# Performance work log

Hardware: AMD Instinct MI355X
Metric: run time of the kernel (lower is better)

## Reference

```python
import jax, jax.numpy as jnp
import numpy as np

NB, BS, NHID, NINP = 6, 200, 1200, 2400  # num_blocks, block_size, nhid, ninp (=2*nhid)
T, B, NTOK = 32, 32, 16000


def _ln(x, g, b):
    mu = x.mean(-1, keepdims=True)
    v = ((x - mu) ** 2).mean(-1, keepdims=True)
    return (x - mu) / jnp.sqrt(v + 1e-5) * g + b


def _attend(q3, k3, v3, wq, wk, wv, wfc, g, b, nh, dk, dv, residual):
    # q3/k3/v3: (B, L, d_model); multi-head scaled-dot attention across blocks
    Bz, L, _ = q3.shape
    qh = (q3 @ wq).reshape(Bz, L, nh, dk)
    kh = (k3 @ wk).reshape(Bz, L, nh, dk)
    vh = (v3 @ wv).reshape(Bz, L, nh, dv)
    att = jnp.einsum('bqhd,bkhd->bhqk', qh, kh) / float(np.sqrt(dk))
    att = jax.nn.softmax(att, axis=-1)
    out = jnp.einsum('bhqk,bkhd->bqhd', att, vh).reshape(Bz, L, nh * dv)
    out = out @ wfc
    if residual:
        out = out + q3
    return _ln(out, g, b)


def setup_inputs() -> dict:
    key = jax.random.key(0)
    ks = jax.random.split(key, 16)
    rn = lambda i, sh, s: jax.random.normal(ks[i], sh, dtype=jnp.float32) * s
    d = {}
    d['tokens'] = jax.random.randint(ks[0], (T, B), 0, NTOK)
    d['h0'] = jnp.zeros((2, B, NHID), jnp.float32)
    d['c0'] = jnp.zeros((2, B, NHID), jnp.float32)
    d['emb_table'] = jax.random.uniform(ks[1], (NTOK, NINP), jnp.float32, -0.1, 0.1)
    d['Wi'] = rn(2, (NB, 4 * BS, NINP), 0.01)
    d['Wh'] = rn(3, (NB, 4 * BS, BS), 0.05)
    d['bih'] = jnp.zeros((NB, 4 * BS), jnp.float32)
    d['bhh'] = jnp.zeros((NB, 4 * BS), jnp.float32)
    d['mq'] = rn(4, (BS, 64), 0.07)
    d['mk'] = rn(5, (BS, 64), 0.07)
    d['mv'] = rn(6, (BS, 64), 0.07)
    d['mfc'] = rn(7, (64, BS), 0.1)
    d['mg'] = jnp.ones((BS,), jnp.float32)
    d['mb'] = jnp.zeros((BS,), jnp.float32)
    d['lq'] = rn(8, (BS, 1600), 0.07)
    d['lk'] = rn(9, (BS, 1600), 0.07)
    d['lv'] = rn(10, (BS, 1600), 0.07)
    d['lfc'] = rn(11, (1600, 2400), 0.02)
    d['lg'] = jnp.ones((2400,), jnp.float32)
    d['lb'] = jnp.zeros((2400,), jnp.float32)
    d['dec_w'] = jax.random.uniform(ks[12], (NTOK, NHID), jnp.float32, -0.1, 0.1)
    d['dec_b'] = jnp.zeros((NTOK,), jnp.float32)
    return d


def reference(tokens, h0, c0, emb_table, Wi, Wh, bih, bhh, mq, mk, mv, mfc, mg, mb,
              lq, lk, lv, lfc, lg, lb, dec_w, dec_b):
    def block_lstm(x, h, c):
        # block-diagonal LSTMCell: k independent cells, per-block input NINP, hidden BS
        Bz = x.shape[0]
        xb = x.reshape(Bz, NB, -1)
        hb = h.reshape(Bz, NB, BS)
        cb = c.reshape(Bz, NB, BS)
        gt = jnp.einsum('bki,kgi->bkg', xb, Wi) + jnp.einsum('bkh,kgh->bkg', hb, Wh) + bih + bhh
        ii, ff, gg, oo = jnp.split(gt, 4, axis=-1)  # torch LSTMCell gate order i,f,g,o
        cn = jax.nn.sigmoid(ff) * cb + jax.nn.sigmoid(ii) * jnp.tanh(gg)
        hn = jax.nn.sigmoid(oo) * jnp.tanh(cn)
        return hn.reshape(Bz, NHID), cn.reshape(Bz, NHID)

    def self_att(h):
        hb = h.reshape(-1, NB, BS)
        hb = _attend(hb, hb, hb, mq, mk, mv, mfc, mg, mb, 4, 16, 16, True)
        return hb.reshape(-1, NHID)

    emb = emb_table[tokens]  # (T, B, NINP)

    def step0(carry, x):
        h, c = carry
        h, c = block_lstm(jnp.tile(x, (1, NB)), h, c)
        h = self_att(h)
        return (h, c), h

    (hf0, cf0), out = jax.lax.scan(step0, (h0[0], c0[0]), emb)

    def step1(carry, x):
        h, c = carry
        q = h.reshape(-1, NB, BS)
        kv = x.reshape(-1, NB, BS)
        inp = _attend(q, kv, kv, lq, lk, lv, lfc, lg, lb, 8, BS, BS, False)  # (B, NB, 2400)
        h, c = block_lstm(inp.reshape(inp.shape[0], -1), h, c)
        h = self_att(h)
        return (h, c), h

    (hf1, cf1), out = jax.lax.scan(step1, (h0[1], c0[1]), out)

    decoded = out @ dec_w.T + dec_b  # (T, B, NTOK)
    return decoded, jnp.stack([hf0, hf1]), jnp.stack([cf0, cf1])
```

## Files before the change

### kernel.cpp

```cpp
#include <hip/hip_runtime.h>
#include <math.h>

#define NBLK 6
#define BS   200
#define NHID 1200
#define NINP 2400
#define TT   32
#define BZ   32
#define NTOK 16000
#define NG   4800
#define ROWS 1024
#define L1D  1600

__device__ __forceinline__ float sigmoidf_(float x) { return 1.0f / (1.0f + expf(-x)); }

template <bool BT>
__global__ __launch_bounds__(256) void gemm128_kernel(
    const float* __restrict__ A, const float* __restrict__ B,
    const float* __restrict__ bias1, const float* __restrict__ bias2,
    float* __restrict__ C, int M, int N, int K, const int* __restrict__ a_idx)
{
    __shared__ __align__(16) float As[8][132];
    __shared__ __align__(16) float Bs[8][132];
    const int tid = threadIdx.x;
    const int tx = tid & 15, ty = tid >> 4;
    const int n0 = blockIdx.x * 128, m0 = blockIdx.y * 128;

    const int la_r = tid >> 1, la_k = (tid & 1) * 4;
    long arow;
    {
        int row = m0 + la_r;
        arow = a_idx ? (long)a_idx[row] * K : (long)row * K;
    }
    float acc[8][8] = {};

    for (int k0 = 0; k0 < K; k0 += 8) {
        {
// ... 38 lines not shown
    for (int i = 0; i < 8; i++) {
        int row = m0 + ty * 4 + (i & 3) + (i >> 2) * 64;
        #pragma unroll
        for (int jg = 0; jg < 2; jg++) {
            int col = n0 + tx * 4 + jg * 64;
            if (col < N) {
                float4 v;
                v.x = acc[i][jg * 4 + 0]; v.y = acc[i][jg * 4 + 1];
                v.z = acc[i][jg * 4 + 2]; v.w = acc[i][jg * 4 + 3];
                if (bias1) {
                    float4 b1 = *(const float4*)&bias1[col];
                    v.x += b1.x; v.y += b1.y; v.z += b1.z; v.w += b1.w;
                }
                if (bias2) {
                    float4 b2 = *(const float4*)&bias2[col];
                    v.x += b2.x; v.y += b2.y; v.z += b2.z; v.w += b2.w;
                }
                *(float4*)&C[(long)row * N + col] = v;
            }
        }
    }
}

__global__ __launch_bounds__(256) void gemm_skp_kernel(
    const float* __restrict__ A, const float* __restrict__ B,
    float* __restrict__ Cp, int M, int N, int K, int KL)
{
    __shared__ __align__(16) float As[8][68];
    __shared__ __align__(16) float Bs[8][68];
    const int tid = threadIdx.x;
    const int tx = tid & 15, ty = tid >> 4;
    const int n0 = blockIdx.x * 64, m0 = blockIdx.y * 64;
    const int z = blockIdx.z;
    const int kbeg = z * KL, kend = kbeg + KL;

    float acc[4][4] = {};

    for (int k0 = kbeg; k0 < kend; k0 += 8) {
        {
            int idx = tid * 2;
            int mm = idx >> 3, kk = idx & 7;
            int row = m0 + mm;
            float2 v = *(const float2*)&A[(long)row * K + k0 + kk];
            As[kk][mm] = v.x;
            As[kk + 1][mm] = v.y;
        }
        {
            int idx = tid * 2;
            int nn = idx & 63, kk = idx >> 6;
            int n = n0 + nn;
            float2 v = make_float2(0.f, 0.f);
            if (n < N) v = *(const float2*)&B[(long)(k0 + kk) * N + n];
            Bs[kk][nn] = v.x;
            Bs[kk][nn + 1] = v.y;
        }
        __syncthreads();
        #pragma unroll
        for (int kk = 0; kk < 8; kk++) {
            const float4 a4 = *(const float4*)&As[kk][ty * 4];
            const float4 b4 = *(const float4*)&Bs[kk][tx * 4];
            const float av[4] = {a4.x, a4.y, a4.z, a4.w};
            const float bv[4] = {b4.x, b4.y, b4.z, b4.w};
            #pragma unroll
            for (int i = 0; i < 4; i++)
                #pragma unroll
                for (int j = 0; j < 4; j++) acc[i][j] += av[i] * bv[j];
        }
        __syncthreads();
    }
    float* Cz = Cp + (long)z * M * N;
    #pragma unroll
    for (int i = 0; i < 4; i++) {
        int row = m0 + ty * 4 + i;
        #pragma unroll
        for (int j = 0; j < 4; j++) {
            int col = n0 + tx * 4 + j;
            if (col < N) Cz[(long)row * N + col] = acc[i][j];
        }
    }
}

__global__ __launch_bounds__(256) void bigb_kernel(
    const float* __restrict__ lq, const float* __restrict__ lk,
    float* __restrict__ BigB)
{
    int id = blockIdx.x * 256 + threadIdx.x;
    if (id >= 320000) return;
    int h = id / 40000, r = id % 40000, cp = r / 200, c = r % 200;
    const float4* a = (const float4*)(lq + (long)c * L1D + h * 200);
    const float4* b = (const float4*)(lk + (long)cp * L1D + h * 200);
    float s0 = 0, s1 = 0, s2 = 0, s3 = 0;
    #pragma unroll 5
    for (int d = 0; d < 50; d++) {
        float4 av = a[d], bv = b[d];
        s0 += av.x * bv.x; s1 += av.y * bv.y; s2 += av.z * bv.z; s3 += av.w * bv.w;
    }
    BigB[(long)cp * L1D + h * 200 + c] = s0 + s1 + s2 + s3;
}

__global__ __launch_bounds__(256) void lstm0_kernel(
    const float* __restrict__ GX,
    const float* __restrict__ hprev,
    float* __restrict__ c_io,
    const float* __restrict__ Wh,
    float* __restrict__ h_out)
{
    __shared__ float h_s[200 * 33];
    const int k = blockIdx.y, jt = blockIdx.x, tid = threadIdx.x;
    for (int idx = tid; idx < 1600; idx += 256) {
        int bb = idx / 50, m4 = idx % 50;
        float4 v = *(const float4*)&hprev[bb * NHID + k * BS + m4 * 4];
        h_s[(m4 * 4 + 0) * 33 + bb] = v.x;
        h_s[(m4 * 4 + 1) * 33 + bb] = v.y;
        h_s[(m4 * 4 + 2) * 33 + bb] = v.z;
        h_s[(m4 * 4 + 3) * 33 + bb] = v.w;
    }
    __syncthreads();
    const int b = tid & 31, jj = tid >> 5;
    const int j = jt * 8 + jj;
    const float* w0 = Wh + (long)(k * 800 + j) * 200;
    const float* w1 = w0 + 200 * 200;
    const float* w2 = w0 + 400 * 200;
    const float* w3 = w0 + 600 * 200;
    float a0 = 0, a1 = 0, a2 = 0, a3 = 0;
    for (int m = 0; m < 200; m += 4) {
        float4 wv0 = *(const float4*)&w0[m];
        float4 wv1 = *(const float4*)&w1[m];
        float4 wv2 = *(const float4*)&w2[m];
        float4 wv3 = *(const float4*)&w3[m];
        float h0v = h_s[(m + 0) * 33 + b];
        float h1v = h_s[(m + 1) * 33 + b];
        float h2v = h_s[(m + 2) * 33 + b];
        float h3v = h_s[(m + 3) * 33 + b];
        a0 += h0v * wv0.x + h1v * wv0.y + h2v * wv0.z + h3v * wv0.w;
        a1 += h0v * wv1.x + h1v * wv1.y + h2v * wv1.z + h3v * wv1.w;
        a2 += h0v * wv2.x + h1v * wv2.y + h2v * wv2.z + h3v * wv2.w;
        a3 += h0v * wv3.x + h1v * wv3.y + h2v * wv3.z + h3v * wv3.w;
    }
    const float* gx = GX + b * NG + k * 800;
    float gi = a0 + gx[j];
    float gf = a1 + gx[200 + j];
    float gg = a2 + gx[400 + j];
    float go = a3 + gx[600 + j];
    int o = b * NHID + k * BS + j;
    float cold = c_io[o];
    float cn = sigmoidf_(gf) * cold + sigmoidf_(gi) * tanhf(gg);
    float hn = sigmoidf_(go) * tanhf(cn);
    c_io[o] = cn;
    h_out[o] = hn;
}

__global__ __launch_bounds__(512) void lstm1_kernel(
    const float* __restrict__ inp, const float* __restrict__ hprev,
    float* __restrict__ c_io, const float* __restrict__ Wi,
    const float* __restrict__ Wh, const float* __restrict__ bih,
    const float* __restrict__ bhh, float* __restrict__ h_out)
{
    __shared__ float h_s[200 * 33];
    __shared__ float x_s[2][100 * 33];
    __shared__ float ps[12][128];
    const int k = blockIdx.y, jt = blockIdx.x, tid = threadIdx.x;
    const int b = tid & 31, jg = (tid >> 5) & 3, kh = tid >> 7;
    const int j = jt * 4 + jg;

    for (int idx = tid; idx < 1600; idx += 512) {
        int bb = idx / 50, m4 = idx % 50;
        float4 v = *(const float4*)&hprev[bb * NHID + k * BS + m4 * 4];
        h_s[(m4 * 4 + 0) * 33 + bb] = v.x;
        h_s[(m4 * 4 + 1) * 33 + bb] = v.y;
        h_s[(m4 * 4 + 2) * 33 + bb] = v.z;
        h_s[(m4 * 4 + 3) * 33 + bb] = v.w;
    }
    for (int idx = tid; idx < 800; idx += 512) {
        int bb = idx / 25, m4 = idx % 25;
        float4 v = *(const float4*)&inp[(long)(bb * 6 + k) * NINP + m4 * 4];
        x_s[0][(m4 * 4 + 0) * 33 + bb] = v.x;
        x_s[0][(m4 * 4 + 1) * 33 + bb] = v.y;
        x_s[0][(m4 * 4 + 2) * 33 + bb] = v.z;
        x_s[0][(m4 * 4 + 3) * 33 + bb] = v.w;
    }

    const float* wi0 = Wi + (long)(k * 800 + j) * NINP;
    const float* wi1 = wi0 + (long)200 * NINP;
    const float* wi2 = wi0 + (long)400 * NINP;
    const float* wi3 = wi0 + (long)600 * NINP;
    float a0 = 0, a1 = 0, a2 = 0, a3 = 0;
    int cur = 0;
    for (int ti = 0; ti < 24; ti++) {
        __syncthreads();
        if (ti + 1 < 24) {
            int kt = (ti + 1) * 100;
            float* xs = x_s[cur ^ 1];
            for (int idx = tid; idx < 800; idx += 512) {
                int bb = idx / 25, m4 = idx % 25;
                float4 v = *(const float4*)&inp[(long)(bb * 6 + k) * NINP + kt + m4 * 4];
                xs[(m4 * 4 + 0) * 33 + bb] = v.x;
                xs[(m4 * 4 + 1) * 33 + bb] = v.y;
                xs[(m4 * 4 + 2) * 33 + bb] = v.z;
                xs[(m4 * 4 + 3) * 33 + bb] = v.w;
            }
        }
        if (ti / 6 == kh) {
            const int kt = ti * 100;
            const float* xs = x_s[cur];
            for (int m = 0; m < 100; m += 4) {
                float4 w0 = *(const float4*)&wi0[kt + m];
                float4 w1 = *(const float4*)&wi1[kt + m];
                float4 w2 = *(const float4*)&wi2[kt + m];
                float4 w3 = *(const float4*)&wi3[kt + m];
                float x0 = xs[(m + 0) * 33 + b];
                float x1 = xs[(m + 1) * 33 + b];
                float x2 = xs[(m + 2) * 33 + b];
                float x3 = xs[(m + 3) * 33 + b];
                a0 += x0 * w0.x + x1 * w0.y + x2 * w0.z + x3 * w0.w;
                a1 += x0 * w1.x + x1 * w1.y + x2 * w1.z + x3 * w1.w;
                a2 += x0 * w2.x + x1 * w2.y + x2 * w2.z + x3 * w2.w;
                a3 += x0 * w3.x + x1 * w3.y + x2 * w3.z + x3 * w3.w;
            }
        }
        cur ^= 1;
    }
    if (kh == 0) {
        const float* w0 = Wh + (long)(k * 800 + j) * 200;
        const float* w1 = w0 + 200 * 200;
        const float* w2 = w0 + 400 * 200;
        const float* w3 = w0 + 600 * 200;
        for (int m = 0; m < 200; m += 4) {
            float4 wv0 = *(const float4*)&w0[m];
            float4 wv1 = *(const float4*)&w1[m];
            float4 wv2 = *(const float4*)&w2[m];
            float4 wv3 = *(const float4*)&w3[m];
            float h0v = h_s[(m + 0) * 33 + b];
            float h1v = h_s[(m + 1) * 33 + b];
            float h2v = h_s[(m + 2) * 33 + b];
            float h3v = h_s[(m + 3) * 33 + b];
            a0 += h0v * wv0.x + h1v * wv0.y + h2v * wv0.z + h3v * wv0.w;
            a1 += h0v * wv1.x + h1v * wv1.y + h2v * wv1.z + h3v * wv1.w;
            a2 += h0v * wv2.x + h1v * wv2.y + h2v * wv2.z + h3v * wv2.w;
            a3 += h0v * wv3.x + h1v * wv3.y + h2v * wv3.z + h3v * wv3.w;
        }
    } else {
        int g = (kh - 1) * 4, t = tid & 127;
        ps[g + 0][t] = a0; ps[g + 1][t] = a1; ps[g + 2][t] = a2; ps[g + 3][t] = a3;
    }
    __syncthreads();
    if (kh == 0) {
        a0 += ps[0][tid] + ps[4][tid] + ps[8][tid];
        a1 += ps[1][tid] + ps[5][tid] + ps[9][tid];
        a2 += ps[2][tid] + ps[6][tid] + ps[10][tid];
        a3 += ps[3][tid] + ps[7][tid] + ps[11][tid];
        int nb = k * 800;
        float gi = a0 + bih[nb + j] + bhh[nb + j];
        float gf = a1 + bih[nb + 200 + j] + bhh[nb + 200 + j];
        float gg = a2 + bih[nb + 400 + j] + bhh[nb + 400 + j];
        float go = a3 + bih[nb + 600 + j] + bhh[nb + 600 + j];
        int o = b * NHID + k * BS + j;
        float cold = c_io[o];
        float cn = sigmoidf_(gf) * cold + sigmoidf_(gi) * tanhf(gg);
        float hn = sigmoidf_(go) * tanhf(cn);
        c_io[o] = cn;
        h_out[o] = hn;
    }
}

__global__ __launch_bounds__(256) void att_small_kernel(
    const float* __restrict__ h_in, float* __restrict__ h_out,
    const float* __restrict__ mq, const float* __restrict__ mk,
    const float* __restrict__ mv, const float* __restrict__ mfc,
    const float* __restrict__ mg, const float* __restrict__ mb)
{
    __shared__ float hb[1200];
    __shared__ float qh[384], kh[384], vh[384];
    __shared__ float att[144];
    __shared__ float outp[384];
    __shared__ float o2[1200];
    __shared__ float mu_s[6], rs_s[6];
    const int b = blockIdx.x, tid = threadIdx.x;
    for (int i = tid; i < 300; i += 256)
        ((float4*)hb)[i] = ((const float4*)(h_in + b * NHID))[i];
    __syncthreads();
    if (tid < 192) {
        int which = tid >> 6, hd = tid & 63;
        const float* Mw = which == 0 ? mq : (which == 1 ? mk : mv);
        float acc[6] = {};
        for (int jx = 0; jx < 200; jx++) {
            float w = Mw[jx * 64 + hd];
            #pragma unroll
            for (int l = 0; l < 6; l++) acc[l] += hb[l * 200 + jx] * w;
        }
        float* dst = which == 0 ? qh : (which == 1 ? kh : vh);
        #pragma unroll
        for (int l = 0; l < 6; l++) dst[l * 64 + hd] = acc[l];
    }
    __syncthreads();
    if (tid < 144) {
        int h = tid / 36, r = tid % 36, q = r / 6, kk = r % 6;
        float s = 0;
        #pragma unroll
        for (int d = 0; d < 16; d++) s += qh[q * 64 + h * 16 + d] * kh[kk * 64 + h * 16 + d];
        att[(h * 6 + q) * 6 + kk] = s * 0.25f;
    }
    __syncthreads();
    if (tid < 24) {
        float* a = &att[tid * 6];
        float mx = a[0];
        for (int i = 1; i < 6; i++) mx = fmaxf(mx, a[i]);
        float sm = 0;
        for (int i = 0; i < 6; i++) { a[i] = expf(a[i] - mx); sm += a[i]; }
        float inv = 1.f / sm;
        for (int i = 0; i < 6; i++) a[i] *= inv;
    }
    __syncthreads();
    for (int id = tid; id < 384; id += 256) {
        int q = id >> 6, hd = id & 63, h = hd >> 4;
        float s = 0;
        #pragma unroll
        for (int kk = 0; kk < 6; kk++) s += att[(h * 6 + q) * 6 + kk] * vh[kk * 64 + hd];
        outp[id] = s;
    }
    __syncthreads();
    if (tid < 200) {
        float acc[6] = {};
        for (int d = 0; d < 64; d++) {
            float w = mfc[d * 200 + tid];
            #pragma unroll
            for (int q = 0; q < 6; q++) acc[q] += outp[q * 64 + d] * w;
        }
// ... 10 lines not shown
            s2 += v.x * v.x + v.y * v.y + v.z * v.z + v.w * v.w;
        }
        float mu = s / 200.f;
        float var = s2 / 200.f - mu * mu;
        mu_s[tid] = mu;
        rs_s[tid] = 1.0f / sqrtf(var + 1e-5f);
    }
    __syncthreads();
    for (int i = tid; i < 300; i += 256) {
        int q = i / 50;
        float4 v = ((float4*)o2)[i];
        float4 g4 = ((const float4*)mg)[i % 50];
        float4 b4 = ((const float4*)mb)[i % 50];
        float mu = mu_s[q], rstd = rs_s[q];
        float4 r;
        r.x = (v.x - mu) * rstd * g4.x + b4.x;
        r.y = (v.y - mu) * rstd * g4.y + b4.y;
        r.z = (v.z - mu) * rstd * g4.z + b4.z;
        r.w = (v.w - mu) * rstd * g4.w + b4.w;
        ((float4*)(h_out + b * NHID))[i] = r;
    }
}

__global__ __launch_bounds__(256) void att1_kernel(
    const float* __restrict__ hp,
    const float* __restrict__ KM,
    const float* __restrict__ VH,
    float* __restrict__ attV)
{
    __shared__ float att[288];
    const int b = blockIdx.x, tid = threadIdx.x;
    const float* qb = hp + b * NHID;
    const float* kb = KM + b * 9600;
    const float* vb = VH + b * 9600;
    for (int id = tid; id < 288; id += 256) {
        int h = id / 36, r = id % 36, q = r / 6, kk = r % 6;
        const float4* qr = (const float4*)(qb + q * 200);
        const float4* kr = (const float4*)(kb + kk * L1D + h * 200);
        float s0 = 0, s1 = 0, s2 = 0, s3 = 0;
        #pragma unroll 5
        for (int d = 0; d < 50; d++) {
            float4 a = qr[d], v = kr[d];
            s0 += a.x * v.x; s1 += a.y * v.y; s2 += a.z * v.z; s3 += a.w * v.w;
        }
        att[(h * 6 + q) * 6 + kk] = (s0 + s1 + s2 + s3) * 0.07071067811865475f;
    }
    __syncthreads();
    if (tid < 48) {
        float* a = &att[tid * 6];
        float mx = a[0];
        for (int i = 1; i < 6; i++) mx = fmaxf(mx, a[i]);
        float sm = 0;
        for (int i = 0; i < 6; i++) { a[i] = expf(a[i] - mx); sm += a[i]; }
        float inv = 1.f / sm;
        for (int i = 0; i < 6; i++) a[i] *= inv;
    }
    __syncthreads();
    for (int hd = tid; hd < L1D; hd += 256) {
        int h = hd / 200;
        float v0 = vb[0 * L1D + hd], v1 = vb[1 * L1D + hd], v2 = vb[2 * L1D + hd];
        float v3 = vb[3 * L1D + hd], v4 = vb[4 * L1D + hd], v5 = vb[5 * L1D + hd];
        #pragma unroll
        for (int q = 0; q < 6; q++) {
            const float* a = &att[(h * 6 + q) * 6];
            float s = a[0] * v0 + a[1] * v1 + a[2] * v2 + a[3] * v3 + a[4] * v4 + a[5] * v5;
            attV[b * 9600 + q * L1D + hd] = s;
        }
    }
}

__global__ __launch_bounds__(256) void ln_sum4_kernel(
    const float* __restrict__ Fp, float* __restrict__ Y,
    const float* __restrict__ g, const float* __restrict__ bta)
{
    __shared__ float rowbuf[2400];
    __shared__ float aw[4], bw[4];
    const int r = blockIdx.x, tid = threadIdx.x;
    const long SL = (long)192 * NINP / 4;
    const float4* f0 = (const float4*)(Fp) + (long)r * (NINP / 4);
    float s = 0, s2 = 0;
    for (int i = tid; i < 600; i += 256) {
        float4 a = f0[i], b2 = f0[SL + i], c = f0[2 * SL + i], d = f0[3 * SL + i];
        float4 v;
        v.x = a.x + b2.x + c.x + d.x;
        v.y = a.y + b2.y + c.y + d.y;
        v.z = a.z + b2.z + c.z + d.z;
        v.w = a.w + b2.w + c.w + d.w;
        ((float4*)rowbuf)[i] = v;
        s += v.x + v.y + v.z + v.w;
        s2 += v.x * v.x + v.y * v.y + v.z * v.z + v.w * v.w;
    }
    for (int off = 32; off; off >>= 1) { s += __shfl_down(s, off); s2 += __shfl_down(s2, off); }
    int wid = tid >> 6, lane = tid & 63;
    if (lane == 0) { aw[wid] = s; bw[wid] = s2; }
    __syncthreads();
    if (tid == 0) {
        float a = 0, a2 = 0;
        for (int w = 0; w < 4; w++) { a += aw[w]; a2 += bw[w]; }
        float mu = a / NINP;
        float var = a2 / NINP - mu * mu;
        aw[0] = mu;
        bw[0] = 1.0f / sqrtf(var + 1e-5f);
    }
    __syncthreads();
    float mu = aw[0], rstd = bw[0];
    for (int i = tid; i < 600; i += 256) {
        float4 v = ((float4*)rowbuf)[i];
        float4 g4 = ((const float4*)g)[i];
        float4 b4 = ((const float4*)bta)[i];
        float4 o;
        o.x = (v.x - mu) * rstd * g4.x + b4.x;
        o.y = (v.y - mu) * rstd * g4.y + b4.y;
        o.z = (v.z - mu) * rstd * g4.z + b4.z;
        o.w = (v.w - mu) * rstd * g4.w + b4.w;
        ((float4*)(Y + (long)r * NINP))[i] = o;
    }
}

extern "C" void kernel_launch(void* const* d_in, const int* in_sizes, int n_in,
                              void* d_out, int out_size, void* d_ws, size_t ws_size,
                              hipStream_t stream)
{
    const int*   tokens = (const int*)  d_in[0];
    const float* h0     = (const float*)d_in[1];
    const float* c0     = (const float*)d_in[2];
    const float* emb    = (const float*)d_in[3];
    const float* Wi     = (const float*)d_in[4];
    const float* Wh     = (const float*)d_in[5];
    const float* bih    = (const float*)d_in[6];
    const float* bhh    = (const float*)d_in[7];
    const float* mq     = (const float*)d_in[8];
    const float* mk     = (const float*)d_in[9];
    const float* mv     = (const float*)d_in[10];
    const float* mfc    = (const float*)d_in[11];
    const float* mg     = (const float*)d_in[12];
    const float* mb     = (const float*)d_in[13];
    const float* lq     = (const float*)d_in[14];
    const float* lk     = (const float*)d_in[15];
    const float* lv     = (const float*)d_in[16];
    const float* lfc    = (const float*)d_in[17];
    const float* lg     = (const float*)d_in[18];
    const float* lb     = (const float*)d_in[19];
    const float* dec_w  = (const float*)d_in[20];
    const float* dec_b  = (const float*)d_in[21];
    float* out = (float*)d_out;

    float* p = (float*)d_ws;
    float* GX0  = p; p += (long)ROWS * NG;
    float* out0 = p; p += (long)ROWS * NHID;
    float* out1 = p; p += (long)ROWS * NHID;
    float* KM   = p; p += (long)ROWS * 6 * L1D;
    float* VH1  = p; p += (long)ROWS * 6 * L1D;
    float* attV = p; p += 192 * L1D;
    float* FCp  = p; p += (long)4 * 192 * NINP;
    float* inp  = p; p += 192 * NINP;
    float* htmp = p; p += BZ * NHID;
    float* cb0  = p; p += BZ * NHID;
    float* cb1  = p; p += BZ * NHID;
    float* BigB = p; p += 200 * L1D;

    const int ST = BZ * NHID;

    hipMemcpyAsync(cb0, c0,      ST * sizeof(float), hipMemcpyDeviceToDevice, stream);
    hipMemcpyAsync(cb1, c0 + ST, ST * sizeof(float), hipMemcpyDeviceToDevice, stream);

    bigb_kernel<<<1250, 256, 0, stream>>>(lq, lk, BigB);

    gemm128_kernel<true><<<dim3(NG / 128 + 1, ROWS / 128), 256, 0, stream>>>(
        emb, Wi, bih, bhh, GX0, ROWS, NG, NINP, tokens);

    for (int t = 0; t < TT; t++) {
        const float* hp = (t == 0) ? h0 : out0 + (t - 1) * ST;
        lstm0_kernel<<<dim3(25, 6), 256, 0, stream>>>(
            GX0 + (long)t * BZ * NG, hp, cb0, Wh, htmp);
        att_small_kernel<<<BZ, 256, 0, stream>>>(htmp, out0 + t * ST, mq, mk, mv, mfc, mg, mb);
    }

    gemm128_kernel<false><<<dim3((L1D + 127) / 128, (ROWS * 6) / 128), 256, 0, stream>>>(
        out0, BigB, nullptr, nullptr, KM, ROWS * 6, L1D, BS, nullptr);
    gemm128_kernel<false><<<dim3((L1D + 127) / 128, (ROWS * 6) / 128), 256, 0, stream>>>(
        out0, lv, nullptr, nullptr, VH1, ROWS * 6, L1D, BS, nullptr);

    for (int t = 0; t < TT; t++) {
        const float* hp = (t == 0) ? h0 + ST : out1 + (t - 1) * ST;
        att1_kernel<<<BZ, 256, 0, stream>>>(
            hp, KM + (long)t * BZ * 6 * L1D, VH1 + (long)t * BZ * 6 * L1D, attV);
        gemm_skp_kernel<<<dim3((NINP + 63) / 64, 3, 4), 256, 0, stream>>>(
            attV, lfc, FCp, 192, NINP, L1D, 400);
        ln_sum4_kernel<<<192, 256, 0, stream>>>(FCp, inp, lg, lb);
        lstm1_kernel<<<dim3(50, 6), 512, 0, stream>>>(inp, hp, cb1, Wi, Wh, bih, bhh, htmp);
        att_small_kernel<<<BZ, 256, 0, stream>>>(htmp, out1 + t * ST, mq, mk, mv, mfc, mg, mb);
    }

    gemm128_kernel<true><<<dim3(NTOK / 128, ROWS / 128), 256, 0, stream>>>(
        out1, dec_w, dec_b, nullptr, out, ROWS, NTOK, NHID, nullptr);

    long off = (long)ROWS * NTOK;
    hipMemcpyAsync(out + off,          out0 + 31 * ST, ST * sizeof(float), hipMemcpyDeviceToDevice, stream);
    hipMemcpyAsync(out + off + ST,     out1 + 31 * ST, ST * sizeof(float), hipMemcpyDeviceToDevice, stream);
    hipMemcpyAsync(out + off + 2 * ST, cb0,            ST * sizeof(float), hipMemcpyDeviceToDevice, stream);
    hipMemcpyAsync(out + off + 3 * ST, cb1,            ST * sizeof(float), hipMemcpyDeviceToDevice, stream);
}
```

Measured before the change: 10.40 ms.

## Fuse per-timestep recurrent kernels into persistent kernels with grid barriers

Replaces the per-timestep launch loops of both LSTM layers with two persistent kernels, one per phase, that step through all timesteps and use an atomic-counter grid barrier between stages. The goal is to remove roughly 224 small kernel launches and their launch gaps. The second-layer LSTM is also rebalanced to 150 blocks of 256 threads, each running the full input reduction, where before it used a 512-thread split-K reduction. This relies on every block being co-resident, or the barrier deadlocks, and blocks that have no work in a stage still pay barrier latency.

```diff
diff --git a/kernel.cpp b/kernel.cpp
--- a/kernel.cpp
+++ b/kernel.cpp
@@ -11,8 +11,27 @@
 #define NG   4800
 #define ROWS 1024
 #define L1D  1600
+#define ST   (BZ*NHID)
 
 __device__ __forceinline__ float sigmoidf_(float x) { return 1.0f / (1.0f + expf(-x)); }
+
+template <int NB>
+__device__ __forceinline__ void gbar(unsigned* bar, unsigned gen) {
+    __syncthreads();
+    if (threadIdx.x == 0) {
+        __threadfence();
+        unsigned old = __hip_atomic_fetch_add(&bar[0], 1u, __ATOMIC_ACQ_REL, __HIP_MEMORY_SCOPE_AGENT);
+        if (old == gen * (unsigned)NB - 1u) {
+            __hip_atomic_store(&bar[16], gen, __ATOMIC_RELEASE, __HIP_MEMORY_SCOPE_AGENT);
+        } else {
+            while (__hip_atomic_load(&bar[16], __ATOMIC_ACQUIRE, __HIP_MEMORY_SCOPE_AGENT) < gen) {
+                __builtin_amdgcn_s_sleep(2);
+            }
+        }
+        __threadfence();
+    }
+    __syncthreads();
+}
 
 template <bool BT>
 __global__ __launch_bounds__(256) void gemm128_kernel(
@@ -97,64 +116,6 @@
     }
 }
 
-__global__ __launch_bounds__(256) void gemm_skp_kernel(
-    const float* __restrict__ A, const float* __restrict__ B,
-    float* __restrict__ Cp, int M, int N, int K, int KL)
-{
-    __shared__ __align__(16) float As[8][68];
-    __shared__ __align__(16) float Bs[8][68];
-    const int tid = threadIdx.x;
-    const int tx = tid & 15, ty = tid >> 4;
-    const int n0 = blockIdx.x * 64, m0 = blockIdx.y * 64;
-    const int z = blockIdx.z;
-    const int kbeg = z * KL, kend = kbeg + KL;
-
-    float acc[4][4] = {};
-
-    for (int k0 = kbeg; k0 < kend; k0 += 8) {
-        {
-            int idx = tid * 2;
-            int mm = idx >> 3, kk = idx & 7;
-            int row = m0 + mm;
-            float2 v = *(const float2*)&A[(long)row * K + k0 + kk];
-            As[kk][mm] = v.x;
-            As[kk + 1][mm] = v.y;
-        }
-        {
-            int idx = tid * 2;
-            int nn = idx & 63, kk = idx >> 6;
-            int n = n0 + nn;
-            float2 v = make_float2(0.f, 0.f);
-            if (n < N) v = *(const float2*)&B[(long)(k0 + kk) * N + n];
-            Bs[kk][nn] = v.x;
-            Bs[kk][nn + 1] = v.y;
-        }
-        __syncthreads();
-        #pragma unroll
-        for (int kk = 0; kk < 8; kk++) {
-            const float4 a4 = *(const float4*)&As[kk][ty * 4];
-            const float4 b4 = *(const float4*)&Bs[kk][tx * 4];
-            const float av[4] = {a4.x, a4.y, a4.z, a4.w};
-            const float bv[4] = {b4.x, b4.y, b4.z, b4.w};
-            #pragma unroll
-            for (int i = 0; i < 4; i++)
-                #pragma unroll
-                for (int j = 0; j < 4; j++) acc[i][j] += av[i] * bv[j];
-        }
-        __syncthreads();
-    }
-    float* Cz = Cp + (long)z * M * N;
-    #pragma unroll
-    for (int i = 0; i < 4; i++) {
-        int row = m0 + ty * 4 + i;
-        #pragma unroll
-        for (int j = 0; j < 4; j++) {
-            int col = n0 + tx * 4 + j;
-            if (col < N) Cz[(long)row * N + col] = acc[i][j];
-        }
-    }
-}
-
 __global__ __launch_bounds__(256) void bigb_kernel(
     const float* __restrict__ lq, const float* __restrict__ lk,
     float* __restrict__ BigB)
@@ -173,184 +134,21 @@
     BigB[(long)cp * L1D + h * 200 + c] = s0 + s1 + s2 + s3;
 }
 
-__global__ __launch_bounds__(256) void lstm0_kernel(
-    const float* __restrict__ GX,
-    const float* __restrict__ hprev,
-    float* __restrict__ c_io,
-    const float* __restrict__ Wh,
-    float* __restrict__ h_out)
+__device__ __forceinline__ void att_small_body(
+    float* smem, const float* h_in, float* h_out, int b,
+    const float* mq, const float* mk, const float* mv, const float* mfc,
+    const float* mg, const float* mb)
 {
-    __shared__ float h_s[200 * 33];
-    const int k = blockIdx.y, jt = blockIdx.x, tid = threadIdx.x;
-    for (int idx = tid; idx < 1600; idx += 256) {
-        int bb = idx / 50, m4 = idx % 50;
-        float4 v = *(const float4*)&hprev[bb * NHID + k * BS + m4 * 4];
-        h_s[(m4 * 4 + 0) * 33 + bb] = v.x;
-        h_s[(m4 * 4 + 1) * 33 + bb] = v.y;
-        h_s[(m4 * 4 + 2) * 33 + bb] = v.z;
-        h_s[(m4 * 4 + 3) * 33 + bb] = v.w;
-    }
-    __syncthreads();
-    const int b = tid & 31, jj = tid >> 5;
-    const int j = jt * 8 + jj;
-    const float* w0 = Wh + (long)(k * 800 + j) * 200;
-    const float* w1 = w0 + 200 * 200;
-    const float* w2 = w0 + 400 * 200;
-    const float* w3 = w0 + 600 * 200;
-    float a0 = 0, a1 = 0, a2 = 0, a3 = 0;
-    for (int m = 0; m < 200; m += 4) {
-        float4 wv0 = *(const float4*)&w0[m];
-        float4 wv1 = *(const float4*)&w1[m];
-        float4 wv2 = *(const float4*)&w2[m];
-        float4 wv3 = *(const float4*)&w3[m];
-        float h0v = h_s[(m + 0) * 33 + b];
-        float h1v = h_s[(m + 1) * 33 + b];
-        float h2v = h_s[(m + 2) * 33 + b];
-        float h3v = h_s[(m + 3) * 33 + b];
-        a0 += h0v * wv0.x + h1v * wv0.y + h2v * wv0.z + h3v * wv0.w;
-        a1 += h0v * wv1.x + h1v * wv1.y + h2v * wv1.z + h3v * wv1.w;
-        a2 += h0v * wv2.x + h1v * wv2.y + h2v * wv2.z + h3v * wv2.w;
-        a3 += h0v * wv3.x + h1v * wv3.y + h2v * wv3.z + h3v * wv3.w;
-    }
-    const float* gx = GX + b * NG + k * 800;
-    float gi = a0 + gx[j];
-    float gf = a1 + gx[200 + j];
-    float gg = a2 + gx[400 + j];
-    float go = a3 + gx[600 + j];
-    int o = b * NHID + k * BS + j;
-    float cold = c_io[o];
-    float cn = sigmoidf_(gf) * cold + sigmoidf_(gi) * tanhf(gg);
-    float hn = sigmoidf_(go) * tanhf(cn);
-    c_io[o] = cn;
-    h_out[o] = hn;
-}
-
-__global__ __launch_bounds__(512) void lstm1_kernel(
-    const float* __restrict__ inp, const float* __restrict__ hprev,
-    float* __restrict__ c_io, const float* __restrict__ Wi,
-    const float* __restrict__ Wh, const float* __restrict__ bih,
-    const float* __restrict__ bhh, float* __restrict__ h_out)
-{
-    __shared__ float h_s[200 * 33];
-    __shared__ float x_s[2][100 * 33];
-    __shared__ float ps[12][128];
-    const int k = blockIdx.y, jt = blockIdx.x, tid = threadIdx.x;
-    const int b = tid & 31, jg = (tid >> 5) & 3, kh = tid >> 7;
-    const int j = jt * 4 + jg;
-
-    for (int idx = tid; idx < 1600; idx += 512) {
-        int bb = idx / 50, m4 = idx % 50;
-        float4 v = *(const float4*)&hprev[bb * NHID + k * BS + m4 * 4];
-        h_s[(m4 * 4 + 0) * 33 + bb] = v.x;
-        h_s[(m4 * 4 + 1) * 33 + bb] = v.y;
-        h_s[(m4 * 4 + 2) * 33 + bb] = v.z;
-        h_s[(m4 * 4 + 3) * 33 + bb] = v.w;
-    }
-    for (int idx = tid; idx < 800; idx += 512) {
-        int bb = idx / 25, m4 = idx % 25;
-        float4 v = *(const float4*)&inp[(long)(bb * 6 + k) * NINP + m4 * 4];
-        x_s[0][(m4 * 4 + 0) * 33 + bb] = v.x;
-        x_s[0][(m4 * 4 + 1) * 33 + bb] = v.y;
-        x_s[0][(m4 * 4 + 2) * 33 + bb] = v.z;
-        x_s[0][(m4 * 4 + 3) * 33 + bb] = v.w;
-    }
-
-    const float* wi0 = Wi + (long)(k * 800 + j) * NINP;
-    const float* wi1 = wi0 + (long)200 * NINP;
-    const float* wi2 = wi0 + (long)400 * NINP;
-    const float* wi3 = wi0 + (long)600 * NINP;
-    float a0 = 0, a1 = 0, a2 = 0, a3 = 0;
-    int cur = 0;
-    for (int ti = 0; ti < 24; ti++) {
-        __syncthreads();
-        if (ti + 1 < 24) {
-            int kt = (ti + 1) * 100;
-            float* xs = x_s[cur ^ 1];
-            for (int idx = tid; idx < 800; idx += 512) {
-                int bb = idx / 25, m4 = idx % 25;
-                float4 v = *(const float4*)&inp[(long)(bb * 6 + k) * NINP + kt + m4 * 4];
-                xs[(m4 * 4 + 0) * 33 + bb] = v.x;
-                xs[(m4 * 4 + 1) * 33 + bb] = v.y;
-                xs[(m4 * 4 + 2) * 33 + bb] = v.z;
-                xs[(m4 * 4 + 3) * 33 + bb] = v.w;
-            }
-        }
-        if (ti / 6 == kh) {
-            const int kt = ti * 100;
-            const float* xs = x_s[cur];
-            for (int m = 0; m < 100; m += 4) {
-                float4 w0 = *(const float4*)&wi0[kt + m];
-                float4 w1 = *(const float4*)&wi1[kt + m];
-                float4 w2 = *(const float4*)&wi2[kt + m];
-                float4 w3 = *(const float4*)&wi3[kt + m];
-                float x0 = xs[(m + 0) * 33 + b];
-                float x1 = xs[(m + 1) * 33 + b];
-                float x2 = xs[(m + 2) * 33 + b];
-                float x3 = xs[(m + 3) * 33 + b];
-                a0 += x0 * w0.x + x1 * w0.y + x2 * w0.z + x3 * w0.w;
-                a1 += x0 * w1.x + x1 * w1.y + x2 * w1.z + x3 * w1.w;
-                a2 += x0 * w2.x + x1 * w2.y + x2 * w2.z + x3 * w2.w;
-                a3 += x0 * w3.x + x1 * w3.y + x2 * w3.z + x3 * w3.w;
-            }
-        }
-        cur ^= 1;
-    }
-    if (kh == 0) {
-        const float* w0 = Wh + (long)(k * 800 + j) * 200;
-        const float* w1 = w0 + 200 * 200;
-        const float* w2 = w0 + 400 * 200;
-        const float* w3 = w0 + 600 * 200;
-        for (int m = 0; m < 200; m += 4) {
-            float4 wv0 = *(const float4*)&w0[m];
-            float4 wv1 = *(const float4*)&w1[m];
-            float4 wv2 = *(const float4*)&w2[m];
-            float4 wv3 = *(const float4*)&w3[m];
-            float h0v = h_s[(m + 0) * 33 + b];
-            float h1v = h_s[(m + 1) * 33 + b];
-            float h2v = h_s[(m + 2) * 33 + b];
-            float h3v = h_s[(m + 3) * 33 + b];
-            a0 += h0v * wv0.x + h1v * wv0.y + h2v * wv0.z + h3v * wv0.w;
-            a1 += h0v * wv1.x + h1v * wv1.y + h2v * wv1.z + h3v * wv1.w;
-            a2 += h0v * wv2.x + h1v * wv2.y + h2v * wv2.z + h3v * wv2.w;
-            a3 += h0v * wv3.x + h1v * wv3.y + h2v * wv3.z + h3v * wv3.w;
-        }
-    } else {
-        int g = (kh - 1) * 4, t = tid & 127;
-        ps[g + 0][t] = a0; ps[g + 1][t] = a1; ps[g + 2][t] = a2; ps[g + 3][t] = a3;
-    }
-    __syncthreads();
-    if (kh == 0) {
-        a0 += ps[0][tid] + ps[4][tid] + ps[8][tid];
-        a1 += ps[1][tid] + ps[5][tid] + ps[9][tid];
-        a2 += ps[2][tid] + ps[6][tid] + ps[10][tid];
-        a3 += ps[3][tid] + ps[7][tid] + ps[11][tid];
-        int nb = k * 800;
-        float gi = a0 + bih[nb + j] + bhh[nb + j];
-        float gf = a1 + bih[nb + 200 + j] + bhh[nb + 200 + j];
-        float gg = a2 + bih[nb + 400 + j] + bhh[nb + 400 + j];
-        float go = a3 + bih[nb + 600 + j] + bhh[nb + 600 + j];
-        int o = b * NHID + k * BS + j;
-        float cold = c_io[o];
-        float cn = sigmoidf_(gf) * cold + sigmoidf_(gi) * tanhf(gg);
-        float hn = sigmoidf_(go) * tanhf(cn);
-        c_io[o] = cn;
-        h_out[o] = hn;
-    }
-}
-
-__global__ __launch_bounds__(256) void att_small_kernel(
-    const float* __restrict__ h_in, float* __restrict__ h_out,
-    const float* __restrict__ mq, const float* __restrict__ mk,
-    const float* __restrict__ mv, const float* __restrict__ mfc,
-    const float* __restrict__ mg, const float* __restrict__ mb)
-{
-    __shared__ float hb[1200];
-    __shared__ float qh[384], kh[384], vh[384];
-    __shared__ float att[144];
-    __shared__ float outp[384];
-    __shared__ float o2[1200];
-    __shared__ float mu_s[6], rs_s[6];
-    const int b = blockIdx.x, tid = threadIdx.x;
+    const int tid = threadIdx.x;
+    float* hb   = smem;
+    float* qh   = smem + 1200;
+    float* kh   = smem + 1584;
+    float* vh   = smem + 1968;
+    float* att  = smem + 2352;
+    float* outp = smem + 2496;
+    float* o2   = smem + 2880;
+    float* mu_s = smem + 4080;
+    float* rs_s = smem + 4088;
     for (int i = tid; i < 300; i += 256)
         ((float4*)hb)[i] = ((const float4*)(h_in + b * NHID))[i];
     __syncthreads();
@@ -377,7 +175,7 @@
     }
     __syncthreads();
     if (tid < 24) {
-        float* a = &att[tid * 6];
+        float* a = att + tid * 6;
         float mx = a[0];
         for (int i = 1; i < 6; i++) mx = fmaxf(mx, a[i]);
         float sm = 0;
@@ -434,98 +232,331 @@
     }
 }
 
-__global__ __launch_bounds__(256) void att1_kernel(
-    const float* __restrict__ hp,
-    const float* __restrict__ KM,
-    const float* __restrict__ VH,
-    float* __restrict__ attV)
+#define GRID_A 160
+__global__ __launch_bounds__(256) void phaseA_kernel(
+    const float* __restrict__ GX0, const float* __restrict__ h0,
+    float* __restrict__ cb0, const float* __restrict__ Wh,
+    float* __restrict__ out0, float* __restrict__ htmp,
+    const float* __restrict__ mq, const float* __restrict__ mk,
+    const float* __restrict__ mv, const float* __restrict__ mfc,
+    const float* __restrict__ mg, const float* __restrict__ mb,
+    unsigned* bar)
 {
-    __shared__ float att[288];
-    const int b = blockIdx.x, tid = threadIdx.x;
-    const float* qb = hp + b * NHID;
-    const float* kb = KM + b * 9600;
-    const float* vb = VH + b * 9600;
-    for (int id = tid; id < 288; id += 256) {
-        int h = id / 36, r = id % 36, q = r / 6, kk = r % 6;
-        const float4* qr = (const float4*)(qb + q * 200);
-        const float4* kr = (const float4*)(kb + kk * L1D + h * 200);
-        float s0 = 0, s1 = 0, s2 = 0, s3 = 0;
-        #pragma unroll 5
-        for (int d = 0; d < 50; d++) {
-            float4 a = qr[d], v = kr[d];
-            s0 += a.x * v.x; s1 += a.y * v.y; s2 += a.z * v.z; s3 += a.w * v.w;
-        }
-        att[(h * 6 + q) * 6 + kk] = (s0 + s1 + s2 + s3) * 0.07071067811865475f;
-    }
-    __syncthreads();
-    if (tid < 48) {
-        float* a = &att[tid * 6];
-        float mx = a[0];
-        for (int i = 1; i < 6; i++) mx = fmaxf(mx, a[i]);
-        float sm = 0;
-        for (int i = 0; i < 6; i++) { a[i] = expf(a[i] - mx); sm += a[i]; }
-        float inv = 1.f / sm;
-        for (int i = 0; i < 6; i++) a[i] *= inv;
-    }
-    __syncthreads();
-    for (int hd = tid; hd < L1D; hd += 256) {
-        int h = hd / 200;
-        float v0 = vb[0 * L1D + hd], v1 = vb[1 * L1D + hd], v2 = vb[2 * L1D + hd];
-        float v3 = vb[3 * L1D + hd], v4 = vb[4 * L1D + hd], v5 = vb[5 * L1D + hd];
-        #pragma unroll
-        for (int q = 0; q < 6; q++) {
-            const float* a = &att[(h * 6 + q) * 6];
-            float s = a[0] * v0 + a[1] * v1 + a[2] * v2 + a[3] * v3 + a[4] * v4 + a[5] * v5;
-            attV[b * 9600 + q * L1D + hd] = s;
-        }
+    __shared__ __align__(16) float smem[13232];
+    const int blk = blockIdx.x, tid = threadIdx.x;
+    unsigned gen = 0;
+    for (int t = 0; t < TT; t++) {
+        const float* hp = (t == 0) ? h0 : out0 + (long)(t - 1) * ST;
+        if (blk < 150) {
+            const int k = blk / 25, jt = blk % 25;
+            float* h_s = smem;
+            for (int idx = tid; idx < 1600; idx += 256) {
+                int bb = idx / 50, m4 = idx % 50;
+                float4 v = *(const float4*)&hp[bb * NHID + k * BS + m4 * 4];
+                h_s[(m4 * 4 + 0) * 33 + bb] = v.x;
+                h_s[(m4 * 4 + 1) * 33 + bb] = v.y;
+                h_s[(m4 * 4 + 2) * 33 + bb] = v.z;
+                h_s[(m4 * 4 + 3) * 33 + bb] = v.w;
+            }
+            __syncthreads();
+            const int b = tid & 31, jj = tid >> 5;
+            const int j = jt * 8 + jj;
+            const float* w0 = Wh + (long)(k * 800 + j) * 200;
+            const float* w1 = w0 + 200 * 200;
+            const float* w2 = w0 + 400 * 200;
+            const float* w3 = w0 + 600 * 200;
+            float a0 = 0, a1 = 0, a2 = 0, a3 = 0;
+            for (int m = 0; m < 200; m += 4) {
+                float4 wv0 = *(const float4*)&w0[m];
+                float4 wv1 = *(const float4*)&w1[m];
+                float4 wv2 = *(const float4*)&w2[m];
+                float4 wv3 = *(const float4*)&w3[m];
+                float h0v = h_s[(m + 0) * 33 + b], h1v = h_s[(m + 1) * 33 + b];
+                float h2v = h_s[(m + 2) * 33 + b], h3v = h_s[(m + 3) * 33 + b];
+                a0 += h0v * wv0.x + h1v * wv0.y + h2v * wv0.z + h3v * wv0.w;
+                a1 += h0v * wv1.x + h1v * wv1.y + h2v * wv1.z + h3v * wv1.w;
+                a2 += h0v * wv2.x + h1v * wv2.y + h2v * wv2.z + h3v * wv2.w;
+                a3 += h0v * wv3.x + h1v * wv3.y + h2v * wv3.z + h3v * wv3.w;
+            }
+            const float* gx = GX0 + (long)t * BZ * NG + b * NG + k * 800;
+            float gi = a0 + gx[j];
+            float gf = a1 + gx[200 + j];
+            float gg = a2 + gx[400 + j];
+            float go = a3 + gx[600 + j];
+            int o = b * NHID + k * BS + j;
+            float cold = cb0[o];
+            float cn = sigmoidf_(gf) * cold + sigmoidf_(gi) * tanhf(gg);
+            float hn = sigmoidf_(go) * tanhf(cn);
+            cb0[o] = cn;
+            htmp[o] = hn;
+        }
+        gbar<GRID_A>(bar, ++gen);
+        if (blk < 32)
+            att_small_body(smem, htmp, out0 + (long)t * ST, blk, mq, mk, mv, mfc, mg, mb);
+        gbar<GRID_A>(bar, ++gen);
     }
 }
 
-__global__ __launch_bounds__(256) void ln_sum4_kernel(
-    const float* __restrict__ Fp, float* __restrict__ Y,
-    const float* __restrict__ g, const float* __restrict__ bta)
+#define GRID_B 256
+__global__ __launch_bounds__(256) void phaseB_kernel(
+    const float* __restrict__ h0, float* __restrict__ cb1,
+    const float* __restrict__ Wi, const float* __restrict__ Wh,
+    const float* __restrict__ bih, const float* __restrict__ bhh,
+    const float* __restrict__ KM, const float* __restrict__ VH1,
+    const float* __restrict__ lfc, const float* __restrict__ lg,
+    const float* __restrict__ lbta,
+    float* __restrict__ out1, float* __restrict__ htmp,
+    float* __restrict__ attV, float* __restrict__ FCp, float* __restrict__ inp,
+    const float* __restrict__ mq, const float* __restrict__ mk,
+    const float* __restrict__ mv, const float* __restrict__ mfc,
+    const float* __restrict__ mg, const float* __restrict__ mb,
+    unsigned* bar)
 {
-    __shared__ float rowbuf[2400];
-    __shared__ float aw[4], bw[4];
-    const int r = blockIdx.x, tid = threadIdx.x;
-    const long SL = (long)192 * NINP / 4;
-    const float4* f0 = (const float4*)(Fp) + (long)r * (NINP / 4);
-    float s = 0, s2 = 0;
-    for (int i = tid; i < 600; i += 256) {
-        float4 a = f0[i], b2 = f0[SL + i], c = f0[2 * SL + i], d = f0[3 * SL + i];
-        float4 v;
-        v.x = a.x + b2.x + c.x + d.x;
-        v.y = a.y + b2.y + c.y + d.y;
-        v.z = a.z + b2.z + c.z + d.z;
-        v.w = a.w + b2.w + c.w + d.w;
-        ((float4*)rowbuf)[i] = v;
-        s += v.x + v.y + v.z + v.w;
-        s2 += v.x * v.x + v.y * v.y + v.z * v.z + v.w * v.w;
-    }
-    for (int off = 32; off; off >>= 1) { s += __shfl_down(s, off); s2 += __shfl_down(s2, off); }
-    int wid = tid >> 6, lane = tid & 63;
-    if (lane == 0) { aw[wid] = s; bw[wid] = s2; }
-    __syncthreads();
-    if (tid == 0) {
-        float a = 0, a2 = 0;
-        for (int w = 0; w < 4; w++) { a += aw[w]; a2 += bw[w]; }
-        float mu = a / NINP;
-        float var = a2 / NINP - mu * mu;
-        aw[0] = mu;
-        bw[0] = 1.0f / sqrtf(var + 1e-5f);
-    }
-    __syncthreads();
-    float mu = aw[0], rstd = bw[0];
-    for (int i = tid; i < 600; i += 256) {
-        float4 v = ((float4*)rowbuf)[i];
-        float4 g4 = ((const float4*)g)[i];
-        float4 b4 = ((const float4*)bta)[i];
-        float4 o;
-        o.x = (v.x - mu) * rstd * g4.x + b4.x;
-        o.y = (v.y - mu) * rstd * g4.y + b4.y;
-        o.z = (v.z - mu) * rstd * g4.z + b4.z;
-        o.w = (v.w - mu) * rstd * g4.w + b4.w;
-        ((float4*)(Y + (long)r * NINP))[i] = o;
+    __shared__ __align__(16) float smem[13232];
+    const int blk = blockIdx.x, tid = threadIdx.x;
+    unsigned gen = 0;
+    for (int t = 0; t < TT; t++) {
+        const float* hp = (t == 0) ? h0 + ST : out1 + (long)(t - 1) * ST;
+        const float* KMt = KM + (long)t * BZ * 6 * L1D;
+        const float* VHt = VH1 + (long)t * BZ * 6 * L1D;
+
+        {
+            const int b = blk >> 3, h = blk & 7;
+            float* attp = smem;
+            float* attr = smem + 80;
+            const float* qb = hp + b * NHID;
+            const float* kb = KMt + (long)b * 9600 + h * 200;
+            if (tid < 72) {
+                int r = tid >> 1, half = tid & 1;
+                int q = r / 6, kk = r % 6;
+                const float4* qr = (const float4*)(qb + q * 200 + half * 100);
+                const float4* kr = (const float4*)(kb + (long)kk * L1D + half * 100);
+                float s0 = 0, s1 = 0, s2 = 0, s3 = 0;
+                #pragma unroll 5
+                for (int d = 0; d < 25; d++) {
+                    float4 a = qr[d], v = kr[d];
+                    s0 += a.x * v.x; s1 += a.y * v.y; s2 += a.z * v.z; s3 += a.w * v.w;
+                }
+                attp[tid] = s0 + s1 + s2 + s3;
+            }
+            __syncthreads();
+            if (tid < 6) {
+                float v[6]; float mx = -1e30f;
+                #pragma unroll
+                for (int kk = 0; kk < 6; kk++) {
+                    float s = (attp[(tid * 6 + kk) * 2] + attp[(tid * 6 + kk) * 2 + 1]) * 0.07071067811865475f;
+                    v[kk] = s; mx = fmaxf(mx, s);
+                }
+                float sm = 0;
+                #pragma unroll
+                for (int kk = 0; kk < 6; kk++) { v[kk] = expf(v[kk] - mx); sm += v[kk]; }
+                float inv = 1.f / sm;
+                #pragma unroll
+                for (int kk = 0; kk < 6; kk++) attr[tid * 6 + kk] = v[kk] * inv;
+            }
+            __syncthreads();
+            if (tid < 200) {
+                int hd = h * 200 + tid;
+                const float* vb = VHt + (long)b * 9600 + hd;
+                float v0 = vb[0], v1 = vb[L1D], v2 = vb[2 * L1D];
+                float v3 = vb[3 * L1D], v4 = vb[4 * L1D], v5 = vb[5 * L1D];
+                #pragma unroll
+                for (int q = 0; q < 6; q++) {
+                    const float* a = attr + q * 6;
+                    attV[(long)b * 9600 + q * L1D + hd] =
+                        a[0] * v0 + a[1] * v1 + a[2] * v2 + a[3] * v3 + a[4] * v4 + a[5] * v5;
+                }
+            }
+        }
+        gbar<GRID_B>(bar, ++gen);
+
+        {
+            float* As = smem;
+            float* Bs = smem + 544;
+            const int tx = tid & 15, ty = tid >> 4;
+            for (int job = blk; job < 456; job += GRID_B) {
+                int z = job / 114, r2 = job % 114, mt = r2 / 38, nt = r2 % 38;
+                int m0 = mt * 64, n0 = nt * 64, kbeg = z * 400;
+                float acc[4][4] = {};
+                for (int k0 = kbeg; k0 < kbeg + 400; k0 += 8) {
+                    {
+                        int idx = tid * 2, mm = idx >> 3, kk = idx & 7;
+                        float2 v = *(const float2*)&attV[(long)(m0 + mm) * L1D + k0 + kk];
+                        As[kk * 68 + mm] = v.x;
+                        As[(kk + 1) * 68 + mm] = v.y;
+                    }
+                    {
+                        int idx = tid * 2, nn = idx & 63, kk = idx >> 6;
+                        int n = n0 + nn;
+                        float2 v = make_float2(0.f, 0.f);
+                        if (n < NINP) v = *(const float2*)&lfc[(long)(k0 + kk) * NINP + n];
+                        Bs[kk * 68 + nn] = v.x;
+                        Bs[kk * 68 + nn + 1] = v.y;
+                    }
+                    __syncthreads();
+                    #pragma unroll
+                    for (int kk = 0; kk < 8; kk++) {
+                        const float4 a4 = *(const float4*)&As[kk * 68 + ty * 4];
+                        const float4 b4 = *(const float4*)&Bs[kk * 68 + tx * 4];
+                        const float av[4] = {a4.x, a4.y, a4.z, a4.w};
+                        const float bv[4] = {b4.x, b4.y, b4.z, b4.w};
+                        #pragma unroll
+                        for (int i = 0; i < 4; i++)
+                            #pragma unroll
+                            for (int jx = 0; jx < 4; jx++) acc[i][jx] += av[i] * bv[jx];
+                    }
+                    __syncthreads();
+                }
+                float* Cz = FCp + (long)z * 192 * NINP;
+                #pragma unroll
+                for (int i = 0; i < 4; i++) {
+                    int row = m0 + ty * 4 + i;
+                    #pragma unroll
+                    for (int jx = 0; jx < 4; jx++) {
+                        int col = n0 + tx * 4 + jx;
+                        if (col < NINP) Cz[(long)row * NINP + col] = acc[i][jx];
+                    }
+                }
+            }
+        }
+        gbar<GRID_B>(bar, ++gen);
+
+        if (blk < 192) {
+            float* rowbuf = smem;
+            float* aw = smem + 2400;
+            float* bw = smem + 2408;
+            const long SL = (long)192 * NINP / 4;
+            const float4* f0 = (const float4*)FCp + (long)blk * (NINP / 4);
+            float s = 0, s2 = 0;
+            for (int i = tid; i < 600; i += 256) {
+                float4 a = f0[i], b2 = f0[SL + i], c = f0[2 * SL + i], d = f0[3 * SL + i];
+                float4 v;
+                v.x = a.x + b2.x + c.x + d.x;
+                v.y = a.y + b2.y + c.y + d.y;
+                v.z = a.z + b2.z + c.z + d.z;
+                v.w = a.w + b2.w + c.w + d.w;
+                ((float4*)rowbuf)[i] = v;
+                s += v.x + v.y + v.z + v.w;
+                s2 += v.x * v.x + v.y * v.y + v.z * v.z + v.w * v.w;
+            }
+            for (int off = 32; off; off >>= 1) { s += __shfl_down(s, off); s2 += __shfl_down(s2, off); }
+            int wid = tid >> 6, lane = tid & 63;
+            if (lane == 0) { aw[wid] = s; bw[wid] = s2; }
+            __syncthreads();
+            if (tid == 0) {
+                float a = 0, a2 = 0;
+                for (int w = 0; w < 4; w++) { a += aw[w]; a2 += bw[w]; }
+                float mu = a / NINP;
+                float var = a2 / NINP - mu * mu;
+                aw[0] = mu;
+                bw[0] = 1.0f / sqrtf(var + 1e-5f);
+            }
+            __syncthreads();
+            float mu = aw[0], rstd = bw[0];
+            for (int i = tid; i < 600; i += 256) {
+                float4 v = ((float4*)rowbuf)[i];
+                float4 g4 = ((const float4*)lg)[i];
+                float4 b4 = ((const float4*)lbta)[i];
+                float4 o;
+                o.x = (v.x - mu) * rstd * g4.x + b4.x;
+                o.y = (v.y - mu) * rstd * g4.y + b4.y;
+                o.z = (v.z - mu) * rstd * g4.z + b4.z;
+                o.w = (v.w - mu) * rstd * g4.w + b4.w;
+                ((float4*)(inp + (long)blk * NINP))[i] = o;
+            }
+        }
+        gbar<GRID_B>(bar, ++gen);
+
+        if (blk < 150) {
+            const int k = blk / 25, jt = blk % 25;
+            float* h_s  = smem;
+            float* x_sA = smem + 6600;
+            float* x_sB = smem + 9900;
+            const int b = tid & 31, jj = tid >> 5;
+            const int j = jt * 8 + jj;
+            for (int idx = tid; idx < 1600; idx += 256) {
+                int bb = idx / 50, m4 = idx % 50;
+                float4 v = *(const float4*)&hp[bb * NHID + k * BS + m4 * 4];
+                h_s[(m4 * 4 + 0) * 33 + bb] = v.x;
+                h_s[(m4 * 4 + 1) * 33 + bb] = v.y;
+                h_s[(m4 * 4 + 2) * 33 + bb] = v.z;
+                h_s[(m4 * 4 + 3) * 33 + bb] = v.w;
+            }
+            for (int idx = tid; idx < 800; idx += 256) {
+                int bb = idx / 25, m4 = idx % 25;
+                float4 v = *(const float4*)&inp[(long)(bb * 6 + k) * NINP + m4 * 4];
+                x_sA[(m4 * 4 + 0) * 33 + bb] = v.x;
+                x_sA[(m4 * 4 + 1) * 33 + bb] = v.y;
+                x_sA[(m4 * 4 + 2) * 33 + bb] = v.z;
+                x_sA[(m4 * 4 + 3) * 33 + bb] = v.w;
+            }
+            const float* wi0 = Wi + (long)(k * 800 + j) * NINP;
+            const float* wi1 = wi0 + (long)200 * NINP;
+            const float* wi2 = wi0 + (long)400 * NINP;
+            const float* wi3 = wi0 + (long)600 * NINP;
+            float a0 = 0, a1 = 0, a2 = 0, a3 = 0;
+            for (int ti = 0; ti < 24; ti++) {
+                float* xs = (ti & 1) ? x_sB : x_sA;
+                float* xn = (ti & 1) ? x_sA : x_sB;
+                __syncthreads();
+                if (ti + 1 < 24) {
+                    int kt = (ti + 1) * 100;
+                    for (int idx = tid; idx < 800; idx += 256) {
+                        int bb = idx / 25, m4 = idx % 25;
+                        float4 v = *(const float4*)&inp[(long)(bb * 6 + k) * NINP + kt + m4 * 4];
+                        xn[(m4 * 4 + 0) * 33 + bb] = v.x;
+                        xn[(m4 * 4 + 1) * 33 + bb] = v.y;
+                        xn[(m4 * 4 + 2) * 33 + bb] = v.z;
+                        xn[(m4 * 4 + 3) * 33 + bb] = v.w;
+                    }
+                }
+                const int kt = ti * 100;
+                for (int m = 0; m < 100; m += 4) {
+                    float4 w0 = *(const float4*)&wi0[kt + m];
+                    float4 w1 = *(const float4*)&wi1[kt + m];
+                    float4 w2 = *(const float4*)&wi2[kt + m];
+                    float4 w3 = *(const float4*)&wi3[kt + m];
+                    float x0 = xs[(m + 0) * 33 + b], x1 = xs[(m + 1) * 33 + b];
+                    float x2 = xs[(m + 2) * 33 + b], x3 = xs[(m + 3) * 33 + b];
+                    a0 += x0 * w0.x + x1 * w0.y + x2 * w0.z + x3 * w0.w;
+                    a1 += x0 * w1.x + x1 * w1.y + x2 * w1.z + x3 * w1.w;
+                    a2 += x0 * w2.x + x1 * w2.y + x2 * w2.z + x3 * w2.w;
+                    a3 += x0 * w3.x + x1 * w3.y + x2 * w3.z + x3 * w3.w;
+                }
+            }
+            const float* w0 = Wh + (long)(k * 800 + j) * 200;
+            const float* w1 = w0 + 200 * 200;
+            const float* w2 = w0 + 400 * 200;
+            const float* w3 = w0 + 600 * 200;
+            for (int m = 0; m < 200; m += 4) {
+                float4 wv0 = *(const float4*)&w0[m];
+                float4 wv1 = *(const float4*)&w1[m];
+                float4 wv2 = *(const float4*)&w2[m];
+                float4 wv3 = *(const float4*)&w3[m];
+                float h0v = h_s[(m + 0) * 33 + b], h1v = h_s[(m + 1) * 33 + b];
+                float h2v = h_s[(m + 2) * 33 + b], h3v = h_s[(m + 3) * 33 + b];
+                a0 += h0v * wv0.x + h1v * wv0.y + h2v * wv0.z + h3v * wv0.w;
+                a1 += h0v * wv1.x + h1v * wv1.y + h2v * wv1.z + h3v * wv1.w;
+                a2 += h0v * wv2.x + h1v * wv2.y + h2v * wv2.z + h3v * wv2.w;
+                a3 += h0v * wv3.x + h1v * wv3.y + h2v * wv3.z + h3v * wv3.w;
+            }
+            int nb2 = k * 800;
+            float gi = a0 + bih[nb2 + j] + bhh[nb2 + j];
+            float gf = a1 + bih[nb2 + 200 + j] + bhh[nb2 + 200 + j];
+            float gg = a2 + bih[nb2 + 400 + j] + bhh[nb2 + 400 + j];
+            float go = a3 + bih[nb2 + 600 + j] + bhh[nb2 + 600 + j];
+            int o = b * NHID + k * BS + j;
+            float cold = cb1[o];
+            float cn = sigmoidf_(gf) * cold + sigmoidf_(gi) * tanhf(gg);
+            float hn = sigmoidf_(go) * tanhf(cn);
+            cb1[o] = cn;
+            htmp[o] = hn;
+        }
+        gbar<GRID_B>(bar, ++gen);
+
+        if (blk < 32)
+            att_small_body(smem, htmp, out1 + (long)t * ST, blk, mq, mk, mv, mfc, mg, mb);
+        gbar<GRID_B>(bar, ++gen);
     }
 }
 
@@ -570,9 +601,9 @@
     float* cb0  = p; p += BZ * NHID;
     float* cb1  = p; p += BZ * NHID;
     float* BigB = p; p += 200 * L1D;
-
-    const int ST = BZ * NHID;
-
+    unsigned* bar = (unsigned*)p; p += 64;
+
+    hipMemsetAsync(bar, 0, 256, stream);
     hipMemcpyAsync(cb0, c0,      ST * sizeof(float), hipMemcpyDeviceToDevice, stream);
     hipMemcpyAsync(cb1, c0 + ST, ST * sizeof(float), hipMemcpyDeviceToDevice, stream);
 
@@ -581,28 +612,17 @@
     gemm128_kernel<true><<<dim3(NG / 128 + 1, ROWS / 128), 256, 0, stream>>>(
         emb, Wi, bih, bhh, GX0, ROWS, NG, NINP, tokens);
 
-    for (int t = 0; t < TT; t++) {
-        const float* hp = (t == 0) ? h0 : out0 + (t - 1) * ST;
-        lstm0_kernel<<<dim3(25, 6), 256, 0, stream>>>(
-            GX0 + (long)t * BZ * NG, hp, cb0, Wh, htmp);
-        att_small_kernel<<<BZ, 256, 0, stream>>>(htmp, out0 + t * ST, mq, mk, mv, mfc, mg, mb);
-    }
+    phaseA_kernel<<<GRID_A, 256, 0, stream>>>(
+        GX0, h0, cb0, Wh, out0, htmp, mq, mk, mv, mfc, mg, mb, bar);
 
     gemm128_kernel<false><<<dim3((L1D + 127) / 128, (ROWS * 6) / 128), 256, 0, stream>>>(
         out0, BigB, nullptr, nullptr, KM, ROWS * 6, L1D, BS, nullptr);
     gemm128_kernel<false><<<dim3((L1D + 127) / 128, (ROWS * 6) / 128), 256, 0, stream>>>(
         out0, lv, nullptr, nullptr, VH1, ROWS * 6, L1D, BS, nullptr);
 
-    for (int t = 0; t < TT; t++) {
-        const float* hp = (t == 0) ? h0 + ST : out1 + (t - 1) * ST;
-        att1_kernel<<<BZ, 256, 0, stream>>>(
-            hp, KM + (long)t * BZ * 6 * L1D, VH1 + (long)t * BZ * 6 * L1D, attV);
-        gemm_skp_kernel<<<dim3((NINP + 63) / 64, 3, 4), 256, 0, stream>>>(
-            attV, lfc, FCp, 192, NINP, L1D, 400);
-        ln_sum4_kernel<<<192, 256, 0, stream>>>(FCp, inp, lg, lb);
-        lstm1_kernel<<<dim3(50, 6), 512, 0, stream>>>(inp, hp, cb1, Wi, Wh, bih, bhh, htmp);
-        att_small_kernel<<<BZ, 256, 0, stream>>>(htmp, out1 + t * ST, mq, mk, mv, mfc, mg, mb);
-    }
+    phaseB_kernel<<<GRID_B, 256, 0, stream>>>(
+        h0, cb1, Wi, Wh, bih, bhh, KM, VH1, lfc, lg, lb,
+        out1, htmp, attV, FCp, inp, mq, mk, mv, mfc, mg, mb, bar + 32);
 
     gemm128_kernel<true><<<dim3(NTOK / 128, ROWS / 128), 256, 0, stream>>>(
         out1, dec_w, dec_b, nullptr, out, ROWS, NTOK, NHID, nullptr);
```

Result: slower. 22.55 ms (+116.8%).
